# Performance work log

Measured on AMD Instinct MI355X. Metric: run time of the kernel, lower is better.

The kernel has to match this reference:

```python
import jax, jax.numpy as jnp
import numpy as np

N_EMBED = 1024
N_HEAD = 16
SEQ = 2048
BATCH = 2


def setup_inputs() -> dict:
    key = jax.random.key(0)
    ks = jax.random.split(key, 5)
    scale_in = 1.0 / np.sqrt(N_EMBED)
    x = jax.random.normal(ks[0], (BATCH, SEQ, N_EMBED), dtype=jnp.float32)
    # attn_proj: Linear(n_embed, 3*n_embed); stored as [in, out] so y = x @ W + b
    W_qkv = jax.random.normal(ks[1], (N_EMBED, 3 * N_EMBED), dtype=jnp.float32) * scale_in
    b_qkv = jax.random.normal(ks[2], (3 * N_EMBED,), dtype=jnp.float32) * 0.01
    # fin_proj: Linear(n_embed, n_embed)
    W_out = jax.random.normal(ks[3], (N_EMBED, N_EMBED), dtype=jnp.float32) * scale_in
    b_out = jax.random.normal(ks[4], (N_EMBED,), dtype=jnp.float32) * 0.01
    return {"x": x, "W_qkv": W_qkv, "b_qkv": b_qkv, "W_out": W_out, "b_out": b_out}


def reference(x, W_qkv, b_qkv, W_out, b_out):
    B, S, D = x.shape
    H = N_HEAD
    hd = D // H
    qkv = x @ W_qkv + b_qkv  # [B, S, 3D]
    q, k, v = jnp.split(qkv, 3, axis=-1)
    # [B, H, S, hd]
    q = q.reshape(B, S, H, hd).transpose(0, 2, 1, 3)
    k = k.reshape(B, S, H, hd).transpose(0, 2, 1, 3)
    v = v.reshape(B, S, H, hd).transpose(0, 2, 1, 3)
    scores = jnp.einsum("bhqd,bhkd->bhqk", q, k) * (1.0 / np.sqrt(hd))
    causal = jnp.tril(jnp.ones((S, S), dtype=bool))  # lower-triangular mask
    scores = jnp.where(causal[None, None], scores, -jnp.inf)
    probs = jax.nn.softmax(scores, axis=-1)
    # dropout is identity in eval mode (inference reference)
    attn = jnp.einsum("bhqk,bhkd->bhqd", probs, v)  # [B, H, S, hd]
    attn = attn.transpose(0, 2, 1, 3).reshape(B, S, D)
    return attn @ W_out + b_out
```

## Files before the change

kernel.cpp:

```cpp
#include <hip/hip_runtime.h>

typedef short bf16x8 __attribute__((ext_vector_type(8)));
typedef short bf16x4 __attribute__((ext_vector_type(4)));
typedef float f32x4 __attribute__((ext_vector_type(4)));
typedef int i32x4 __attribute__((ext_vector_type(4)));
typedef int i32x2 __attribute__((ext_vector_type(2)));

#define MFMA16x16x32(a, b, c) __builtin_amdgcn_mfma_f32_16x16x32_bf16(a, b, c, 0, 0, 0)
#define TRR(dst, a) asm volatile("ds_read_b64_tr_b16 %0, %1" : "=v"(dst) : "v"(a))

__device__ __forceinline__ unsigned short f2bf(float f) {
  union { float f; unsigned u; } v; v.f = f;
  unsigned u = v.u + 0x7FFFu + ((v.u >> 16) & 1u);
  return (unsigned short)(u >> 16);
}

__device__ __forceinline__ unsigned cvtpk(float lo, float hi) {
  unsigned r;
  asm("v_cvt_pk_bf16_f32 %0, %1, %2" : "=v"(r) : "v"(lo), "v"(hi));
  return r;
}

__device__ __forceinline__ float max3f(float a, float b, float c) {
  float d;
  asm("v_max3_f32 %0, %1, %2, %3" : "=v"(d) : "v"(a), "v"(b), "v"(c));
  return d;
}

__device__ __forceinline__ void gload16(const void* g, void* l) {
  __builtin_amdgcn_global_load_lds((const __attribute__((address_space(1))) void*)g,
                                   (__attribute__((address_space(3))) void*)l, 16, 0, 0);
}

__device__ __forceinline__ unsigned ldsoff(const void* p) {
  return (unsigned)(unsigned long long)(const __attribute__((address_space(3))) void*)p;
}

__global__ __launch_bounds__(256) void conv_bf16(const float* __restrict__ in,
                                                 unsigned short* __restrict__ out, int n8) {
  int i = blockIdx.x * 256 + threadIdx.x;
  if (i >= n8) return;
  const float4* p = reinterpret_cast<const float4*>(in + (long)i * 8);
  float4 a = p[0], b = p[1];
  i32x4 o;
  o[0] = cvtpk(a.x, a.y); o[1] = cvtpk(a.z, a.w);
  o[2] = cvtpk(b.x, b.y); o[3] = cvtpk(b.z, b.w);
  *reinterpret_cast<i32x4*>(out + (long)i * 8) = o;
}

__global__ __launch_bounds__(256) void trans_f32_bf16(const float* __restrict__ W,
                                                      unsigned short* __restrict__ Wt,
                                                      int K, int N) {
  __shared__ float tile[32][33];
  int n0 = blockIdx.x << 5, k0 = blockIdx.y << 5;
  int tx = threadIdx.x, ty = threadIdx.y;
#pragma unroll
  for (int i = 0; i < 32; i += 8)
    tile[ty + i][tx] = W[(long)(k0 + ty + i) * N + n0 + tx];
  __syncthreads();
#pragma unroll
  for (int i = 0; i < 32; i += 8)
    Wt[(long)(n0 + ty + i) * K + k0 + tx] = f2bf(tile[tx][ty + i]);
}

template <int BF16OUT>
__global__ __launch_bounds__(256) void gemm_bt(const unsigned short* __restrict__ A,
                                               const unsigned short* __restrict__ Bt,
                                               const float* __restrict__ bias,
                                               void* __restrict__ Cv,
                                               int M, int N, int K) {
  __shared__ __align__(128) unsigned short As[8192];
  __shared__ __align__(128) unsigned short Bs[8192];
  int t = threadIdx.x;
  int w = t >> 6, l = t & 63;
  int g = l >> 4, m16 = l & 15;
  int wr = w >> 1, wc = w & 1;
  int nwg = gridDim.x * gridDim.y;
  int f = blockIdx.y * gridDim.x + blockIdx.x;
  int q8 = nwg >> 3;
  int s = (f & 7) * q8 + (f >> 3);
  int bx = s % gridDim.x, by = s / gridDim.x;
  long am0 = (long)by << 7;
  long bn0 = (long)bx << 7;
  f32x4 acc[4][4];
#pragma unroll
  for (int i = 0; i < 4; ++i)
#pragma unroll
    for (int j = 0; j < 4; ++j) acc[i][j] = (f32x4){0.f, 0.f, 0.f, 0.f};

  for (int k0 = 0; k0 < K; k0 += 64) {
#pragma unroll
    for (int i = 0; i < 4; ++i) {
      int seg = i * 4 + w;
      int flat = (seg << 9) + (l << 3);
      int r_ = flat >> 6, c_ = flat & 63;
      gload16(A + (am0 + r_) * K + k0 + c_, &As[seg << 9]);
      gload16(Bt + (bn0 + r_) * K + k0 + c_, &Bs[seg << 9]);
    }
    asm volatile("s_waitcnt vmcnt(0)" ::: "memory");
    __syncthreads();
#pragma unroll
    for (int kk = 0; kk < 2; ++kk) {
      bf16x8 af[4], bfr[4];
#pragma unroll
      for (int im = 0; im < 4; ++im)
        af[im] = *(const bf16x8*)&As[((wr << 6) + (im << 4) + m16) * 64 + (kk << 5) + (g << 3)];
#pragma unroll
      for (int in = 0; in < 4; ++in)
        bfr[in] = *(const bf16x8*)&Bs[((wc << 6) + (in << 4) + m16) * 64 + (kk << 5) + (g << 3)];
      __builtin_amdgcn_s_setprio(1);
#pragma unroll
      for (int im = 0; im < 4; ++im)
#pragma unroll
        for (int in = 0; in < 4; ++in)
          acc[im][in] = MFMA16x16x32(af[im], bfr[in], acc[im][in]);
      __builtin_amdgcn_s_setprio(0);
    }
    __syncthreads();
  }

#pragma unroll
  for (int im = 0; im < 4; ++im) {
#pragma unroll
    for (int in = 0; in < 4; ++in) {
      long col = bn0 + (wc << 6) + (in << 4) + m16;
      float bval = bias[col];
#pragma unroll
      for (int r = 0; r < 4; ++r) {
        long row = am0 + (wr << 6) + (im << 4) + (g << 2) + r;
        float v = acc[im][in][r] + bval;
        if (BF16OUT)
          ((unsigned short*)Cv)[row * N + col] = f2bf(v);
        else
          ((float*)Cv)[row * N + col] = v;
      }
    }
  }
}

__global__ __launch_bounds__(256, 3) void attn_fwd(const unsigned short* __restrict__ qkv,
                                                   unsigned short* __restrict__ out) {
  const int D3 = 3072;
  const float C1 = 0.18033688f;
  const float THR = 11.5415603f;
  __shared__ __align__(128) unsigned short Ks[2][4096];
  __shared__ __align__(128) unsigned short Vs[2][4096];
  int b = blockIdx.x >> 4, h = blockIdx.x & 15;
  int yy = blockIdx.y;
  int qt = (yy & 1) ? (31 - (yy >> 1)) : (yy >> 1);
  int t = threadIdx.x;
  int w = t >> 6, l = t & 63;
  int g = l >> 4, m16 = l & 15;
  long base = (long)b * 2048 * D3;
  const unsigned short* kbase = qkv + base + 1024 + h * 64;
  const unsigned short* vbase = qkv + base + 2048 + h * 64;

  int l8 = l >> 3, sc = l & 7;
  int kof = (w * 8 + l8) * D3 + ((sc ^ l8) << 3);
  int s0 = w * 8 + l8;
  int vof = ((s0 & 15) * 4 + (sc >> 1)) * D3 + ((s0 >> 4) << 4) + ((sc & 1) << 3);
  const f32x4 zero4 = (f32x4){0.f, 0.f, 0.f, 0.f};

  int qrow = (qt << 6) + (w << 4) + m16;
  const unsigned short* qp = qkv + base + (long)qrow * D3 + h * 64;
  bf16x8 qf0 = *(const bf16x8*)(qp + g * 8);
  bf16x8 qf1 = *(const bf16x8*)(qp + 32 + g * 8);

  f32x4 O[4];
#pragma unroll
  for (int d = 0; d < 4; ++d) O[d] = zero4;
  f32x4 lsv = zero4;
  float m2 = -1e30f;
  int nt = qt + 1;

  gload16(kbase + kof, &Ks[0][w << 9]);
  gload16(kbase + 32 * D3 + kof, &Ks[0][2048 + (w << 9)]);
  gload16(vbase + vof, &Vs[0][w << 9]);
  gload16(vbase + vof + 32, &Vs[0][2048 + (w << 9)]);

  int buf = 0;
  for (int ss = 0; ss < nt; ++ss) {
    asm volatile("s_waitcnt vmcnt(0)" ::: "memory");
    __syncthreads();
    if (ss + 1 < nt) {
      long off = (long)(ss + 1) * 64 * D3;
      gload16(kbase + off + kof, &Ks[buf ^ 1][w << 9]);
      gload16(kbase + off + 32 * D3 + kof, &Ks[buf ^ 1][2048 + (w << 9)]);
      gload16(vbase + off + vof, &Vs[buf ^ 1][w << 9]);
      gload16(vbase + off + vof + 32, &Vs[buf ^ 1][2048 + (w << 9)]);
    }

    unsigned va = ldsoff(&Vs[buf][0]) + (g << 7) + (m16 << 3);
    bf16x4 t0[4], t1[4], t2[4], t3[4];
#pragma unroll
    for (int d = 0; d < 4; ++d) {
      unsigned a = va + (d << 11);
      TRR(t0[d], a);
      TRR(t1[d], a + 512);
      TRR(t2[d], a + 1024);
      TRR(t3[d], a + 1536);
    }
    const char* kbuf = (const char*)&Ks[buf][0];
    int swz = m16 & 7;
    f32x4 st[4];
    __builtin_amdgcn_s_setprio(1);
#pragma unroll
    for (int T = 0; T < 4; ++T) {
      const char* rp = kbuf + (((T << 4) + m16) << 7);
      bf16x8 kf0 = *(const bf16x8*)(rp + ((g ^ swz) << 4));
      bf16x8 kf1 = *(const bf16x8*)(rp + (((4 + g) ^ swz) << 4));
      st[T] = MFMA16x16x32(kf0, qf0, zero4);
      st[T] = MFMA16x16x32(kf1, qf1, st[T]);
    }
    __builtin_amdgcn_s_setprio(0);

    if (ss == nt - 1) {
      int rq = qrow - (ss << 6);
#pragma unroll
      for (int T = 0; T < 4; ++T)
#pragma unroll
        for (int r = 0; r < 4; ++r)
          if ((T << 4) + (g << 2) + r > rq) st[T][r] = -3e38f;
    }
    float tm[4];
#pragma unroll
    for (int T = 0; T < 4; ++T)
      tm[T] = max3f(fmaxf(st[T][0], st[T][1]), st[T][2], st[T][3]);
    float tmax = fmaxf(max3f(tm[0], tm[1], tm[2]), tm[3]);
    tmax = fmaxf(tmax, __shfl_xor(tmax, 16));
    tmax = fmaxf(tmax, __shfl_xor(tmax, 32));
    float tsc2 = tmax * C1;
    bool skip = __all(tsc2 <= m2 + THR);
    float mnew2 = skip ? m2 : fmaxf(m2, tsc2);
    float p[4][4];
    f32x4 ts4 = zero4;
#pragma unroll
    for (int T = 0; T < 4; ++T)
#pragma unroll
      for (int r = 0; r < 4; ++r) {
        float e = __builtin_amdgcn_exp2f(fmaf(st[T][r], C1, -mnew2));
        p[T][r] = e;
        ts4[r] += e;
      }
    if (!skip) {
      float alpha = __builtin_amdgcn_exp2f(m2 - mnew2);
      lsv *= alpha;
#pragma unroll
      for (int d = 0; d < 4; ++d) O[d] *= alpha;
      m2 = mnew2;
    }
    lsv += ts4;

    i32x4 w0, w1;
    w0[0] = cvtpk(p[0][0], p[0][1]); w0[1] = cvtpk(p[0][2], p[0][3]);
    w0[2] = cvtpk(p[1][0], p[1][1]); w0[3] = cvtpk(p[1][2], p[1][3]);
    w1[0] = cvtpk(p[2][0], p[2][1]); w1[1] = cvtpk(p[2][2], p[2][3]);
    w1[2] = cvtpk(p[3][0], p[3][1]); w1[3] = cvtpk(p[3][2], p[3][3]);
    bf16x8 pb0 = __builtin_bit_cast(bf16x8, w0);
    bf16x8 pb1 = __builtin_bit_cast(bf16x8, w1);

    asm volatile("s_waitcnt lgkmcnt(0)" ::: "memory");
    __builtin_amdgcn_sched_barrier(0);

    bf16x8 vfA[4], vfB[4];
#pragma unroll
    for (int d = 0; d < 4; ++d) {
      vfA[d] = __builtin_shufflevector(t0[d], t1[d], 0, 1, 2, 3, 4, 5, 6, 7);
      vfB[d] = __builtin_shufflevector(t2[d], t3[d], 0, 1, 2, 3, 4, 5, 6, 7);
    }
    __builtin_amdgcn_s_setprio(1);
#pragma unroll
    for (int d = 0; d < 4; ++d) {
      O[d] = MFMA16x16x32(vfA[d], pb0, O[d]);
      O[d] = MFMA16x16x32(vfB[d], pb1, O[d]);
    }
    __builtin_amdgcn_s_setprio(0);
    buf ^= 1;
  }

  float s = (lsv[0] + lsv[1]) + (lsv[2] + lsv[3]);
  s += __shfl_xor(s, 16);
  s += __shfl_xor(s, 32);
  float inv = 1.0f / s;
  unsigned short* op = out + (long)(b * 2048 + qrow) * 1024 + h * 64;
#pragma unroll
  for (int d = 0; d < 4; ++d) {
    i32x2 pk;
    pk[0] = (int)cvtpk(O[d][0] * inv, O[d][1] * inv);
    pk[1] = (int)cvtpk(O[d][2] * inv, O[d][3] * inv);
    *reinterpret_cast<i32x2*>(op + (d << 4) + (g << 2)) = pk;
  }
}

extern "C" void kernel_launch(void* const* d_in, const int* in_sizes, int n_in,
                              void* d_out, int out_size, void* d_ws, size_t ws_size,
                              hipStream_t stream) {
  const float* x     = (const float*)d_in[0];
  const float* W_qkv = (const float*)d_in[1];
  const float* b_qkv = (const float*)d_in[2];
  const float* W_out = (const float*)d_in[3];
  const float* b_out = (const float*)d_in[4];

  char* ws = (char*)d_ws;
  unsigned short* xb    = (unsigned short*)ws;
  unsigned short* wqkvT = (unsigned short*)(ws + (8l << 20));
  unsigned short* woutT = (unsigned short*)(ws + (14l << 20));
  unsigned short* qkv   = (unsigned short*)(ws + (16l << 20));

  conv_bf16<<<2048, 256, 0, stream>>>(x, xb, 524288);
  trans_f32_bf16<<<dim3(96, 32), dim3(32, 8), 0, stream>>>(W_qkv, wqkvT, 1024, 3072);
  trans_f32_bf16<<<dim3(32, 32), dim3(32, 8), 0, stream>>>(W_out, woutT, 1024, 1024);
  gemm_bt<1><<<dim3(24, 32), 256, 0, stream>>>(xb, wqkvT, b_qkv, (void*)qkv, 4096, 3072, 1024);
  attn_fwd<<<dim3(32, 32), 256, 0, stream>>>(qkv, xb);
  gemm_bt<0><<<dim3(8, 32), 256, 0, stream>>>(xb, woutT, b_out, d_out, 4096, 1024, 1024);
}
```

Baseline: 118.0 us.

## Double-buffer GEMM shared-memory tiles with K-step of 32 to overlap loads

Splits the GEMM's shared-memory A/B tiles into two ping-pong buffers of half the K-depth (32 instead of 64). The next K-slice's global-to-LDS loads are issued before computing on the current slice, and one barrier per iteration replaces two. The aim is to hide global load latency behind the MFMA work. In exchange, the loop runs twice as many iterations with less compute per barrier, and the narrower 32-element LDS rows may change bank-conflict behaviour.

```diff
diff --git a/kernel.cpp b/kernel.cpp
--- a/kernel.cpp
+++ b/kernel.cpp
@@ -69,8 +69,8 @@
                                                const float* __restrict__ bias,
                                                void* __restrict__ Cv,
                                                int M, int N, int K) {
-  __shared__ __align__(128) unsigned short As[8192];
-  __shared__ __align__(128) unsigned short Bs[8192];
+  __shared__ __align__(128) unsigned short As[2][4096];
+  __shared__ __align__(128) unsigned short Bs[2][4096];
   int t = threadIdx.x;
   int w = t >> 6, l = t & 63;
   int g = l >> 4, m16 = l & 15;
@@ -82,41 +82,49 @@
   int bx = s % gridDim.x, by = s / gridDim.x;
   long am0 = (long)by << 7;
   long bn0 = (long)bx << 7;
+
+  int seg0 = w, seg1 = 4 + w;
+  int fl0 = (seg0 << 9) + (l << 3), fl1 = (seg1 << 9) + (l << 3);
+  int r0 = fl0 >> 5, c0 = fl0 & 31;
+  int r1 = fl1 >> 5, c1 = fl1 & 31;
+
   f32x4 acc[4][4];
 #pragma unroll
   for (int i = 0; i < 4; ++i)
 #pragma unroll
     for (int j = 0; j < 4; ++j) acc[i][j] = (f32x4){0.f, 0.f, 0.f, 0.f};
 
-  for (int k0 = 0; k0 < K; k0 += 64) {
-#pragma unroll
-    for (int i = 0; i < 4; ++i) {
-      int seg = i * 4 + w;
-      int flat = (seg << 9) + (l << 3);
-      int r_ = flat >> 6, c_ = flat & 63;
-      gload16(A + (am0 + r_) * K + k0 + c_, &As[seg << 9]);
-      gload16(Bt + (bn0 + r_) * K + k0 + c_, &Bs[seg << 9]);
-    }
+  gload16(A + (am0 + r0) * K + c0, &As[0][seg0 << 9]);
+  gload16(A + (am0 + r1) * K + c1, &As[0][seg1 << 9]);
+  gload16(Bt + (bn0 + r0) * K + c0, &Bs[0][seg0 << 9]);
+  gload16(Bt + (bn0 + r1) * K + c1, &Bs[0][seg1 << 9]);
+
+  int buf = 0;
+  for (int k0 = 0; k0 < K; k0 += 32) {
     asm volatile("s_waitcnt vmcnt(0)" ::: "memory");
     __syncthreads();
-#pragma unroll
-    for (int kk = 0; kk < 2; ++kk) {
-      bf16x8 af[4], bfr[4];
-#pragma unroll
-      for (int im = 0; im < 4; ++im)
-        af[im] = *(const bf16x8*)&As[((wr << 6) + (im << 4) + m16) * 64 + (kk << 5) + (g << 3)];
+    if (k0 + 32 < K) {
+      int kn = k0 + 32;
+      gload16(A + (am0 + r0) * K + kn + c0, &As[buf ^ 1][seg0 << 9]);
+      gload16(A + (am0 + r1) * K + kn + c1, &As[buf ^ 1][seg1 << 9]);
+      gload16(Bt + (bn0 + r0) * K + kn + c0, &Bs[buf ^ 1][seg0 << 9]);
+      gload16(Bt + (bn0 + r1) * K + kn + c1, &Bs[buf ^ 1][seg1 << 9]);
+    }
+    bf16x8 af[4], bfr[4];
+#pragma unroll
+    for (int im = 0; im < 4; ++im)
+      af[im] = *(const bf16x8*)&As[buf][((wr << 6) + (im << 4) + m16) * 32 + (g << 3)];
+#pragma unroll
+    for (int in = 0; in < 4; ++in)
+      bfr[in] = *(const bf16x8*)&Bs[buf][((wc << 6) + (in << 4) + m16) * 32 + (g << 3)];
+    __builtin_amdgcn_s_setprio(1);
+#pragma unroll
+    for (int im = 0; im < 4; ++im)
 #pragma unroll
       for (int in = 0; in < 4; ++in)
-        bfr[in] = *(const bf16x8*)&Bs[((wc << 6) + (in << 4) + m16) * 64 + (kk << 5) + (g << 3)];
-      __builtin_amdgcn_s_setprio(1);
-#pragma unroll
-      for (int im = 0; im < 4; ++im)
-#pragma unroll
-        for (int in = 0; in < 4; ++in)
-          acc[im][in] = MFMA16x16x32(af[im], bfr[in], acc[im][in]);
-      __builtin_amdgcn_s_setprio(0);
-    }
-    __syncthreads();
+        acc[im][in] = MFMA16x16x32(af[im], bfr[in], acc[im][in]);
+    __builtin_amdgcn_s_setprio(0);
+    buf ^= 1;
   }
 
 #pragma unroll
```

After: 116.0 us. About the same (-1.7%).
